# Kernel optimization log

Measured on AMD Instinct MI355X. Metric: run time of the kernel, lower is better.

Reference implementation:

```python
import jax, jax.numpy as jnp
import numpy as np

N = 100000
E = 1600000
F = 64
OUT = 7

def setup_inputs() -> dict:
    key = jax.random.key(0)
    k1, k2, k3, k4, k5 = jax.random.split(key, 5)
    x = jax.random.normal(k1, (N, F), dtype=jnp.float32)
    edge_index = jax.random.randint(k2, (2, E), 0, N, dtype=jnp.int64)
    W_l = jax.random.normal(k3, (F, OUT), dtype=jnp.float32) / np.sqrt(F)
    b_l = jax.random.normal(k4, (OUT,), dtype=jnp.float32) * 0.01
    W_r = jax.random.normal(k5, (F, OUT), dtype=jnp.float32) / np.sqrt(F)
    return {"x": x, "edge_index": edge_index, "W_l": W_l, "b_l": b_l, "W_r": W_r}

def reference(x, edge_index, W_l, b_l, W_r):
    # PyG SAGEConv (mean aggr): out = lin_l(mean_{j in N(i)} x_j) + lin_r(x_i), then relu
    src, dst = edge_index[0], edge_index[1]
    msgs = x[src]                                            # [E, F] gather
    agg = jax.ops.segment_sum(msgs, dst, num_segments=N)     # [N, F]
    cnt = jax.ops.segment_sum(jnp.ones((E,), dtype=x.dtype), dst, num_segments=N)
    mean = agg / jnp.maximum(cnt, 1.0)[:, None]              # isolated nodes -> 0
    out = mean @ W_l + b_l + x @ W_r                         # [N, 7]
    return jax.nn.relu(out)
```

## Files before the change

kernel.cpp:

```cpp
#include <hip/hip_runtime.h>

#define NN 100000
#define NE 1600000
#define FIN 64
#define FOUT 7

#define BSH 9
#define NBK 196
#define PBLK 2000
#define PTH  256
#define EPB  800
#define EPT  4
#define NCOPY 4
#define NCTR (NBK * NCOPY)
#define ROWS 200
#define SPLIT 2
#define RPS (PBLK / SPLIT)
#define ATH 1024
#define CAPR 8
#define OVCAP 256
#define SCAP 4608
#define PROJB 391
#define INVALID 0xFFFFFFFFu

__device__ __forceinline__ unsigned bf16r(float f) {
    unsigned u = __float_as_uint(f);
    return (u + 0x7fffu + ((u >> 16) & 1u)) >> 16;
}
__device__ __forceinline__ float bflo(unsigned u) { return __uint_as_float(u << 16); }
__device__ __forceinline__ float bfhi(unsigned u) { return __uint_as_float(u & 0xffff0000u); }

__global__ __launch_bounds__(256) void proj_kernel(
    const float* __restrict__ x, const float* __restrict__ Wl,
    const float* __restrict__ bl, const float* __restrict__ Wr,
    unsigned* __restrict__ z, float* __restrict__ outself, int n)
{
    int i = blockIdx.x * blockDim.x + threadIdx.x;
    if (i >= n) return;

    float al[FOUT], ar[FOUT];
#pragma unroll
    for (int j = 0; j < FOUT; ++j) { al[j] = 0.f; ar[j] = 0.f; }

    const float4* xr = (const float4*)(x + (size_t)i * FIN);
#pragma unroll
    for (int kk = 0; kk < FIN / 4; ++kk) {
        float4 xv = xr[kk];
        float v[4] = {xv.x, xv.y, xv.z, xv.w};
#pragma unroll
        for (int c = 0; c < 4; ++c) {
            int k = kk * 4 + c;
#pragma unroll
            for (int j = 0; j < FOUT; ++j) {
                al[j] = fmaf(v[c], Wl[k * FOUT + j], al[j]);
                ar[j] = fmaf(v[c], Wr[k * FOUT + j], ar[j]);
            }
        }
    }

    uint4 pk;
    pk.x = bf16r(al[0]) | (bf16r(al[1]) << 16);
    pk.y = bf16r(al[2]) | (bf16r(al[3]) << 16);
    pk.z = bf16r(al[4]) | (bf16r(al[5]) << 16);
    pk.w = bf16r(al[6]);
    ((uint4*)z)[i] = pk;

    float* o = outself + (size_t)i * FOUT;
#pragma unroll
    for (int j = 0; j < FOUT; ++j)
        o[j] = ar[j] + bl[j];
}

__global__ __launch_bounds__(PTH) void part_kernel(
    const int* __restrict__ eg, unsigned* __restrict__ part,
    unsigned short* __restrict__ offs)
{
    __shared__ unsigned st_cnt[NCTR];
    __shared__ unsigned st_start[NCTR];
    __shared__ unsigned wsum[NCOPY];

    const int t    = threadIdx.x;
    const int e0   = (int)blockIdx.x * EPB;
    const int lane = t & 63;
    const int wv   = t >> 6;

    for (int b = t; b < NCTR; b += PTH) st_cnt[b] = 0;
    __syncthreads();

    unsigned held[EPT], hcr[EPT];
#pragma unroll
    for (int j = 0; j < EPT; ++j) {
        int k = t + j * PTH;
        if (k < EPB) {
            unsigned s = (unsigned)eg[e0 + k];
            unsigned d = (unsigned)eg[NE + e0 + k];
            unsigned cidx = (d >> BSH) * NCOPY + wv;
            unsigned r = atomicAdd(&st_cnt[cidx], 1u);
            held[j] = ((d & 511u) << 17) | s;
            hcr[j]  = (cidx << 10) | r;
        } else hcr[j] = INVALID;
    }
    __syncthreads();

    {
        unsigned c[4], sum = 0;
#pragma unroll
        for (int q = 0; q < 4; ++q) {
            int idx = 4 * t + q;
            c[q] = (idx < NCTR) ? st_cnt[idx] : 0u;
            sum += c[q];
        }
        unsigned inc = sum;
#pragma unroll
        for (int off = 1; off < 64; off <<= 1) {
            unsigned v = (unsigned)__shfl_up((int)inc, off, 64);
            if (lane >= off) inc += v;
        }
        if (lane == 63) wsum[wv] = inc;
        __syncthreads();
        if (t == 0) {
            unsigned run = 0;
#pragma unroll
            for (int w = 0; w < NCOPY; ++w) { unsigned tmp = wsum[w]; wsum[w] = run; run += tmp; }
        }
        __syncthreads();
        unsigned base = wsum[wv] + inc - sum;
#pragma unroll
        for (int q = 0; q < 4; ++q) {
            int idx = 4 * t + q;
            if (idx < NCTR) st_start[idx] = base;
            base += c[q];
        }
    }
    __syncthreads();

    if (t <= NBK)
        offs[(size_t)blockIdx.x * ROWS + t] =
            (unsigned short)((t == NBK) ? EPB : st_start[t * NCOPY]);

    unsigned* pr = part + (size_t)blockIdx.x * EPB;
#pragma unroll
    for (int j = 0; j < EPT; ++j) {
        if (hcr[j] != INVALID) {
            unsigned cidx = hcr[j] >> 10, r = hcr[j] & 0x3FFu;
            pr[st_start[cidx] + r] = held[j];
        }
    }
}

__global__ __launch_bounds__(ATH) void acc_kernel(
    const unsigned short* __restrict__ offs, const unsigned* __restrict__ part,
    const unsigned* __restrict__ zb, float* __restrict__ partial)
{
    __shared__ unsigned s_cnt[512];
    __shared__ unsigned s_start[512];
    __shared__ unsigned sstage[SCAP];
    __shared__ float    lacc[512 * 8];
    __shared__ unsigned ovf[2 * OVCAP];
    __shared__ unsigned novf;
    __shared__ unsigned wtot[8];

    const int t = threadIdx.x;
    const int k = blockIdx.x >> 1;
    const int s = blockIdx.x & 1;

    if (t < 512) s_cnt[t] = 0;
    if (t == 0) novf = 0;
    __syncthreads();

    unsigned rbase = 0, len = 0;
    if (t < RPS) {
        unsigned r = (unsigned)(s * RPS + t);
        unsigned o0 = offs[(size_t)r * ROWS + k];
        unsigned o1 = offs[(size_t)r * ROWS + k + 1];
        len   = o1 - o0;
        rbase = r * EPB + o0;
    }

    unsigned hsrc[CAPR], hnr[CAPR];
#pragma unroll
    for (int j = 0; j < CAPR; ++j) {
        if (j < (int)len) {
            unsigned e = part[rbase + j];
            unsigned node = e >> 17;
            unsigned r = atomicAdd(&s_cnt[node], 1u);
            hsrc[j] = e & 0x1FFFFu;
            hnr[j]  = (node << 16) | r;
        } else hnr[j] = INVALID;
    }
    for (int j = CAPR; j < (int)len; ++j) {
        unsigned e = part[rbase + j];
        unsigned node = e >> 17;
        unsigned r = atomicAdd(&s_cnt[node], 1u);
        unsigned p = atomicAdd(&novf, 1u);
        if (p < OVCAP) {
            ovf[2 * p]     = (node << 16) | r;
            ovf[2 * p + 1] = e & 0x1FFFFu;
        }
    }
    __syncthreads();

    unsigned cval = 0, inc = 0;
    if (t < 512) {
        cval = s_cnt[t];
        inc = cval;
#pragma unroll
        for (int off = 1; off < 64; off <<= 1) {
            unsigned v = (unsigned)__shfl_up((int)inc, off, 64);
            if ((t & 63) >= off) inc += v;
        }
        if ((t & 63) == 63) wtot[t >> 6] = inc;
    }
    __syncthreads();
    if (t == 0) {
        unsigned run = 0;
#pragma unroll
        for (int w = 0; w < 8; ++w) { unsigned tmp = wtot[w]; wtot[w] = run; run += tmp; }
    }
    __syncthreads();
    if (t < 512) s_start[t] = wtot[t >> 6] + inc - cval;
    __syncthreads();

#pragma unroll
    for (int j = 0; j < CAPR; ++j) {
        if (hnr[j] != INVALID) {
            unsigned node = hnr[j] >> 16, r = hnr[j] & 0xffffu;
            unsigned p = s_start[node] + r;
            if (p < SCAP) sstage[p] = hsrc[j];
        }
    }
    for (unsigned q = t; q < min(novf, (unsigned)OVCAP); q += ATH) {
        unsigned nr = ovf[2 * q], src = ovf[2 * q + 1];
        unsigned p = s_start[nr >> 16] + (nr & 0xffffu);
        if (p < SCAP) sstage[p] = src;
    }
    __syncthreads();

    unsigned node = t & 511u;
    unsigned half = (unsigned)t >> 9;
    unsigned deg  = s_cnt[node];
    unsigned base = s_start[node];
    unsigned lo = half ? (deg >> 1) : 0u;
    unsigned hi = half ? deg : (deg >> 1);

    float a0 = 0.f, a1 = 0.f, a2 = 0.f, a3 = 0.f, a4 = 0.f, a5 = 0.f, a6 = 0.f;
    for (unsigned j = lo; j < hi && base + j < SCAP; ++j) {
        unsigned src = sstage[base + j];
        uint4 zr = ((const uint4*)zb)[src];
        a0 += bflo(zr.x); a1 += bfhi(zr.x);
        a2 += bflo(zr.y); a3 += bfhi(zr.y);
        a4 += bflo(zr.z); a5 += bfhi(zr.z);
        a6 += bflo(zr.w);
    }

    if (half) {
        float* L = &lacc[node * 8];
        *(float4*)(L)     = make_float4(a0, a1, a2, a3);
        *(float4*)(L + 4) = make_float4(a4, a5, a6, 0.f);
    }
    __syncthreads();

    if (!half) {
        const float* L = &lacc[node * 8];
        a0 += L[0]; a1 += L[1]; a2 += L[2]; a3 += L[3];
        a4 += L[4]; a5 += L[5]; a6 += L[6];
        float* pp = partial + ((size_t)blockIdx.x * 512 + node) * 8;
        *(float4*)(pp)     = make_float4(a0, a1, a2, a3);
        *(float4*)(pp + 4) = make_float4(a4, a5, a6, (float)deg);
    }
}

__global__ __launch_bounds__(256) void merge_kernel(
    const float* __restrict__ partial, float* __restrict__ out, int n)
{
    int i = blockIdx.x * blockDim.x + threadIdx.x;
    if (i >= n) return;
    int k = i >> BSH;
    int node = i & 511;

    float s0 = 0.f, s1 = 0.f, s2 = 0.f, s3 = 0.f, s4 = 0.f, s5 = 0.f, s6 = 0.f, cn = 0.f;
#pragma unroll
    for (int s = 0; s < SPLIT; ++s) {
        const float4* p = (const float4*)(partial + ((size_t)(k * SPLIT + s) * 512 + node) * 8);
        float4 a = p[0], b = p[1];
        s0 += a.x; s1 += a.y; s2 += a.z; s3 += a.w;
        s4 += b.x; s5 += b.y; s6 += b.z; cn += b.w;
    }
    float r = 1.0f / fmaxf(cn, 1.0f);
    float* o = out + (size_t)i * FOUT;
    o[0] = fmaxf(fmaf(s0, r, o[0]), 0.f);
    o[1] = fmaxf(fmaf(s1, r, o[1]), 0.f);
    o[2] = fmaxf(fmaf(s2, r, o[2]), 0.f);
    o[3] = fmaxf(fmaf(s3, r, o[3]), 0.f);
    o[4] = fmaxf(fmaf(s4, r, o[4]), 0.f);
    o[5] = fmaxf(fmaf(s5, r, o[5]), 0.f);
    o[6] = fmaxf(fmaf(s6, r, o[6]), 0.f);
}

extern "C" void kernel_launch(void* const* d_in, const int* in_sizes, int n_in,
                              void* d_out, int out_size, void* d_ws, size_t ws_size,
                              hipStream_t stream) {
    const float* x   = (const float*)d_in[0];
    const int*   edg = (const int*)d_in[1];
    const float* Wl  = (const float*)d_in[2];
    const float* bl  = (const float*)d_in[3];
    const float* Wr  = (const float*)d_in[4];
    float* out = (float*)d_out;

    unsigned*       z       = (unsigned*)d_ws;
    unsigned*       part    = z + (size_t)NN * 4;
    unsigned short* offs    = (unsigned short*)(part + (size_t)NE);
    float*          partial = (float*)(offs + (size_t)PBLK * ROWS);

    proj_kernel<<<PROJB, 256, 0, stream>>>(x, Wl, bl, Wr, z, out, NN);
    part_kernel<<<PBLK, PTH, 0, stream>>>(edg, part, offs);
    acc_kernel<<<NBK * SPLIT, ATH, 0, stream>>>(offs, part, z, partial);
    merge_kernel<<<(NN + 255) / 256, 256, 0, stream>>>(partial, out, NN);
}
```

Measured before the change: 127.1 us.

## Fuse four kernels into one persistent kernel with grid-wide barriers

Merges the projection, partition, accumulate and merge kernels into a single persistent kernel of 256 blocks of 1024 threads, with atomic-counter grid barriers between phases. This removes three kernel launches and their inter-kernel gaps. The partition step now stages edges in shared memory and writes them out coalesced as uint4. The accumulate split goes from 2 to 4 per bucket, with one thread per node and no half-split reduction. The cost is lower parallelism in each phase and spin-wait barrier overhead. The barrier also relies on all 256 blocks being co-resident, and it adds a memset launch.

```diff
diff --git a/kernel.cpp b/kernel.cpp
--- a/kernel.cpp
+++ b/kernel.cpp
@@ -7,20 +7,19 @@
 
 #define BSH 9
 #define NBK 196
-#define PBLK 2000
-#define PTH  256
+#define NREG 2000
 #define EPB  800
-#define EPT  4
+#define ROWS 200
 #define NCOPY 4
 #define NCTR (NBK * NCOPY)
-#define ROWS 200
-#define SPLIT 2
-#define RPS (PBLK / SPLIT)
-#define ATH 1024
+#define SPLIT 4
+#define NTASK (NBK * SPLIT)
+#define RPS (NREG / SPLIT)
 #define CAPR 8
 #define OVCAP 256
-#define SCAP 4608
-#define PROJB 391
+#define SCAP 2560
+#define BLKS 256
+#define TH 1024
 #define INVALID 0xFFFFFFFFu
 
 __device__ __forceinline__ unsigned bf16r(float f) {
@@ -30,271 +29,250 @@
 __device__ __forceinline__ float bflo(unsigned u) { return __uint_as_float(u << 16); }
 __device__ __forceinline__ float bfhi(unsigned u) { return __uint_as_float(u & 0xffff0000u); }
 
-__global__ __launch_bounds__(256) void proj_kernel(
-    const float* __restrict__ x, const float* __restrict__ Wl,
-    const float* __restrict__ bl, const float* __restrict__ Wr,
-    unsigned* __restrict__ z, float* __restrict__ outself, int n)
+__device__ __forceinline__ void gbarrier(int* cnt, int* gen) {
+    __syncthreads();
+    if (threadIdx.x == 0) {
+        int g = __hip_atomic_load(gen, __ATOMIC_ACQUIRE, __HIP_MEMORY_SCOPE_AGENT);
+        int a = __hip_atomic_fetch_add(cnt, 1, __ATOMIC_ACQ_REL, __HIP_MEMORY_SCOPE_AGENT);
+        if (a == BLKS - 1) {
+            __hip_atomic_store(cnt, 0, __ATOMIC_RELAXED, __HIP_MEMORY_SCOPE_AGENT);
+            __hip_atomic_fetch_add(gen, 1, __ATOMIC_ACQ_REL, __HIP_MEMORY_SCOPE_AGENT);
+        } else {
+            while (__hip_atomic_load(gen, __ATOMIC_ACQUIRE, __HIP_MEMORY_SCOPE_AGENT) == g)
+                __builtin_amdgcn_s_sleep(2);
+        }
+    }
+    __syncthreads();
+}
+
+__global__ __launch_bounds__(TH) void mega_kernel(
+    const int* __restrict__ eg, const float* __restrict__ x,
+    const float* __restrict__ Wl, const float* __restrict__ bl,
+    const float* __restrict__ Wr, unsigned* __restrict__ z,
+    unsigned* __restrict__ part, unsigned short* __restrict__ offs,
+    float* __restrict__ partial, float* __restrict__ out, int* __restrict__ bar)
 {
-    int i = blockIdx.x * blockDim.x + threadIdx.x;
-    if (i >= n) return;
-
-    float al[FOUT], ar[FOUT];
-#pragma unroll
-    for (int j = 0; j < FOUT; ++j) { al[j] = 0.f; ar[j] = 0.f; }
-
-    const float4* xr = (const float4*)(x + (size_t)i * FIN);
-#pragma unroll
-    for (int kk = 0; kk < FIN / 4; ++kk) {
-        float4 xv = xr[kk];
-        float v[4] = {xv.x, xv.y, xv.z, xv.w};
-#pragma unroll
-        for (int c = 0; c < 4; ++c) {
-            int k = kk * 4 + c;
-#pragma unroll
-            for (int j = 0; j < FOUT; ++j) {
-                al[j] = fmaf(v[c], Wl[k * FOUT + j], al[j]);
-                ar[j] = fmaf(v[c], Wr[k * FOUT + j], ar[j]);
-            }
-        }
-    }
-
-    uint4 pk;
-    pk.x = bf16r(al[0]) | (bf16r(al[1]) << 16);
-    pk.y = bf16r(al[2]) | (bf16r(al[3]) << 16);
-    pk.z = bf16r(al[4]) | (bf16r(al[5]) << 16);
-    pk.w = bf16r(al[6]);
-    ((uint4*)z)[i] = pk;
-
-    float* o = outself + (size_t)i * FOUT;
-#pragma unroll
-    for (int j = 0; j < FOUT; ++j)
-        o[j] = ar[j] + bl[j];
-}
-
-__global__ __launch_bounds__(PTH) void part_kernel(
-    const int* __restrict__ eg, unsigned* __restrict__ part,
-    unsigned short* __restrict__ offs)
-{
-    __shared__ unsigned st_cnt[NCTR];
-    __shared__ unsigned st_start[NCTR];
-    __shared__ unsigned wsum[NCOPY];
+    __shared__ unsigned s_cnt[NCTR];
+    __shared__ unsigned s_start[NCTR];
+    __shared__ unsigned sstage[SCAP];
+    __shared__ unsigned ovf[2 * OVCAP];
+    __shared__ unsigned novf;
+    __shared__ unsigned wtot[16];
 
     const int t    = threadIdx.x;
-    const int e0   = (int)blockIdx.x * EPB;
     const int lane = t & 63;
-    const int wv   = t >> 6;
-
-    for (int b = t; b < NCTR; b += PTH) st_cnt[b] = 0;
-    __syncthreads();
-
-    unsigned held[EPT], hcr[EPT];
-#pragma unroll
-    for (int j = 0; j < EPT; ++j) {
-        int k = t + j * PTH;
-        if (k < EPB) {
-            unsigned s = (unsigned)eg[e0 + k];
-            unsigned d = (unsigned)eg[NE + e0 + k];
-            unsigned cidx = (d >> BSH) * NCOPY + wv;
-            unsigned r = atomicAdd(&st_cnt[cidx], 1u);
-            held[j] = ((d & 511u) << 17) | s;
-            hcr[j]  = (cidx << 10) | r;
-        } else hcr[j] = INVALID;
-    }
-    __syncthreads();
 
     {
-        unsigned c[4], sum = 0;
-#pragma unroll
-        for (int q = 0; q < 4; ++q) {
-            int idx = 4 * t + q;
-            c[q] = (idx < NCTR) ? st_cnt[idx] : 0u;
-            sum += c[q];
-        }
-        unsigned inc = sum;
-#pragma unroll
-        for (int off = 1; off < 64; off <<= 1) {
-            unsigned v = (unsigned)__shfl_up((int)inc, off, 64);
-            if (lane >= off) inc += v;
-        }
-        if (lane == 63) wsum[wv] = inc;
+        int i = (int)blockIdx.x * TH + t;
+        if (i < NN) {
+            float al[FOUT], ar[FOUT];
+#pragma unroll
+            for (int j = 0; j < FOUT; ++j) { al[j] = 0.f; ar[j] = 0.f; }
+            const float4* xr = (const float4*)(x + (size_t)i * FIN);
+#pragma unroll
+            for (int kk = 0; kk < FIN / 4; ++kk) {
+                float4 xv = xr[kk];
+                float v[4] = {xv.x, xv.y, xv.z, xv.w};
+#pragma unroll
+                for (int c = 0; c < 4; ++c) {
+                    int k = kk * 4 + c;
+#pragma unroll
+                    for (int j = 0; j < FOUT; ++j) {
+                        al[j] = fmaf(v[c], Wl[k * FOUT + j], al[j]);
+                        ar[j] = fmaf(v[c], Wr[k * FOUT + j], ar[j]);
+                    }
+                }
+            }
+            uint4 pk;
+            pk.x = bf16r(al[0]) | (bf16r(al[1]) << 16);
+            pk.y = bf16r(al[2]) | (bf16r(al[3]) << 16);
+            pk.z = bf16r(al[4]) | (bf16r(al[5]) << 16);
+            pk.w = bf16r(al[6]);
+            ((uint4*)z)[i] = pk;
+            float* o = out + (size_t)i * FOUT;
+#pragma unroll
+            for (int j = 0; j < FOUT; ++j) o[j] = ar[j] + bl[j];
+        }
+    }
+
+    for (int r = blockIdx.x; r < NREG; r += BLKS) {
+        for (int i = t; i < NCTR; i += TH) s_cnt[i] = 0;
+        __syncthreads();
+
+        unsigned held = 0, hcr = INVALID;
+        if (t < EPB) {
+            unsigned s = (unsigned)eg[r * EPB + t];
+            unsigned d = (unsigned)eg[NE + r * EPB + t];
+            unsigned cidx = (d >> BSH) * NCOPY + ((t >> 6) & 3);
+            unsigned rk = atomicAdd(&s_cnt[cidx], 1u);
+            held = ((d & 511u) << 17) | s;
+            hcr  = (cidx << 10) | rk;
+        }
+        __syncthreads();
+
+        unsigned c0 = 0, c1 = 0, p = 0, inc = 0;
+        if (t < 512) {
+            unsigned i0 = 2 * t, i1 = 2 * t + 1;
+            c0 = (i0 < NCTR) ? s_cnt[i0] : 0u;
+            c1 = (i1 < NCTR) ? s_cnt[i1] : 0u;
+            p = c0 + c1; inc = p;
+#pragma unroll
+            for (int off = 1; off < 64; off <<= 1) {
+                unsigned v = (unsigned)__shfl_up((int)inc, off, 64);
+                if (lane >= off) inc += v;
+            }
+            if (lane == 63) wtot[t >> 6] = inc;
+        }
         __syncthreads();
         if (t == 0) {
             unsigned run = 0;
 #pragma unroll
-            for (int w = 0; w < NCOPY; ++w) { unsigned tmp = wsum[w]; wsum[w] = run; run += tmp; }
-        }
-        __syncthreads();
-        unsigned base = wsum[wv] + inc - sum;
-#pragma unroll
-        for (int q = 0; q < 4; ++q) {
-            int idx = 4 * t + q;
-            if (idx < NCTR) st_start[idx] = base;
-            base += c[q];
-        }
-    }
-    __syncthreads();
-
-    if (t <= NBK)
-        offs[(size_t)blockIdx.x * ROWS + t] =
-            (unsigned short)((t == NBK) ? EPB : st_start[t * NCOPY]);
-
-    unsigned* pr = part + (size_t)blockIdx.x * EPB;
-#pragma unroll
-    for (int j = 0; j < EPT; ++j) {
-        if (hcr[j] != INVALID) {
-            unsigned cidx = hcr[j] >> 10, r = hcr[j] & 0x3FFu;
-            pr[st_start[cidx] + r] = held[j];
-        }
-    }
-}
-
-__global__ __launch_bounds__(ATH) void acc_kernel(
-    const unsigned short* __restrict__ offs, const unsigned* __restrict__ part,
-    const unsigned* __restrict__ zb, float* __restrict__ partial)
-{
-    __shared__ unsigned s_cnt[512];
-    __shared__ unsigned s_start[512];
-    __shared__ unsigned sstage[SCAP];
-    __shared__ float    lacc[512 * 8];
-    __shared__ unsigned ovf[2 * OVCAP];
-    __shared__ unsigned novf;
-    __shared__ unsigned wtot[8];
-
-    const int t = threadIdx.x;
-    const int k = blockIdx.x >> 1;
-    const int s = blockIdx.x & 1;
-
-    if (t < 512) s_cnt[t] = 0;
-    if (t == 0) novf = 0;
-    __syncthreads();
-
-    unsigned rbase = 0, len = 0;
-    if (t < RPS) {
-        unsigned r = (unsigned)(s * RPS + t);
-        unsigned o0 = offs[(size_t)r * ROWS + k];
-        unsigned o1 = offs[(size_t)r * ROWS + k + 1];
-        len   = o1 - o0;
-        rbase = r * EPB + o0;
-    }
-
-    unsigned hsrc[CAPR], hnr[CAPR];
-#pragma unroll
-    for (int j = 0; j < CAPR; ++j) {
-        if (j < (int)len) {
+            for (int w = 0; w < 8; ++w) { unsigned tmp = wtot[w]; wtot[w] = run; run += tmp; }
+        }
+        __syncthreads();
+        if (t < 512) {
+            unsigned base = wtot[t >> 6] + inc - p;
+            unsigned i0 = 2 * t, i1 = 2 * t + 1;
+            if (i0 < NCTR) s_start[i0] = base;
+            if (i1 < NCTR) s_start[i1] = base + c0;
+        }
+        __syncthreads();
+
+        if (t <= NBK)
+            offs[(size_t)r * ROWS + t] =
+                (unsigned short)((t == NBK) ? EPB : s_start[t * NCOPY]);
+        if (hcr != INVALID)
+            sstage[s_start[hcr >> 10] + (hcr & 1023u)] = held;
+        __syncthreads();
+
+        uint4* pg = (uint4*)(part + (size_t)r * EPB);
+        if (t < EPB / 4) pg[t] = ((const uint4*)sstage)[t];
+        __syncthreads();
+    }
+
+    gbarrier(bar, bar + 16);
+
+    for (int task = blockIdx.x; task < NTASK; task += BLKS) {
+        const int k  = task >> 2;
+        const int sp = task & 3;
+
+        if (t < 512) s_cnt[t] = 0;
+        if (t == 0) novf = 0;
+        __syncthreads();
+
+        unsigned rbase = 0, len = 0;
+        if (t < RPS) {
+            unsigned r = (unsigned)(sp * RPS + t);
+            unsigned o0 = offs[(size_t)r * ROWS + k];
+            unsigned o1 = offs[(size_t)r * ROWS + k + 1];
+            len   = o1 - o0;
+            rbase = r * EPB + o0;
+        }
+
+        unsigned hsrc[CAPR], hnr[CAPR];
+#pragma unroll
+        for (int j = 0; j < CAPR; ++j) {
+            if (j < (int)len) {
+                unsigned e = part[rbase + j];
+                unsigned node = e >> 17;
+                unsigned rk = atomicAdd(&s_cnt[node], 1u);
+                hsrc[j] = e & 0x1FFFFu;
+                hnr[j]  = (node << 16) | rk;
+            } else hnr[j] = INVALID;
+        }
+        for (int j = CAPR; j < (int)len; ++j) {
             unsigned e = part[rbase + j];
             unsigned node = e >> 17;
-            unsigned r = atomicAdd(&s_cnt[node], 1u);
-            hsrc[j] = e & 0x1FFFFu;
-            hnr[j]  = (node << 16) | r;
-        } else hnr[j] = INVALID;
-    }
-    for (int j = CAPR; j < (int)len; ++j) {
-        unsigned e = part[rbase + j];
-        unsigned node = e >> 17;
-        unsigned r = atomicAdd(&s_cnt[node], 1u);
-        unsigned p = atomicAdd(&novf, 1u);
-        if (p < OVCAP) {
-            ovf[2 * p]     = (node << 16) | r;
-            ovf[2 * p + 1] = e & 0x1FFFFu;
-        }
-    }
-    __syncthreads();
-
-    unsigned cval = 0, inc = 0;
-    if (t < 512) {
-        cval = s_cnt[t];
-        inc = cval;
-#pragma unroll
-        for (int off = 1; off < 64; off <<= 1) {
-            unsigned v = (unsigned)__shfl_up((int)inc, off, 64);
-            if ((t & 63) >= off) inc += v;
-        }
-        if ((t & 63) == 63) wtot[t >> 6] = inc;
-    }
-    __syncthreads();
-    if (t == 0) {
-        unsigned run = 0;
-#pragma unroll
-        for (int w = 0; w < 8; ++w) { unsigned tmp = wtot[w]; wtot[w] = run; run += tmp; }
-    }
-    __syncthreads();
-    if (t < 512) s_start[t] = wtot[t >> 6] + inc - cval;
-    __syncthreads();
-
-#pragma unroll
-    for (int j = 0; j < CAPR; ++j) {
-        if (hnr[j] != INVALID) {
-            unsigned node = hnr[j] >> 16, r = hnr[j] & 0xffffu;
-            unsigned p = s_start[node] + r;
-            if (p < SCAP) sstage[p] = hsrc[j];
-        }
-    }
-    for (unsigned q = t; q < min(novf, (unsigned)OVCAP); q += ATH) {
-        unsigned nr = ovf[2 * q], src = ovf[2 * q + 1];
-        unsigned p = s_start[nr >> 16] + (nr & 0xffffu);
-        if (p < SCAP) sstage[p] = src;
-    }
-    __syncthreads();
-
-    unsigned node = t & 511u;
-    unsigned half = (unsigned)t >> 9;
-    unsigned deg  = s_cnt[node];
-    unsigned base = s_start[node];
-    unsigned lo = half ? (deg >> 1) : 0u;
-    unsigned hi = half ? deg : (deg >> 1);
-
-    float a0 = 0.f, a1 = 0.f, a2 = 0.f, a3 = 0.f, a4 = 0.f, a5 = 0.f, a6 = 0.f;
-    for (unsigned j = lo; j < hi && base + j < SCAP; ++j) {
-        unsigned src = sstage[base + j];
-        uint4 zr = ((const uint4*)zb)[src];
-        a0 += bflo(zr.x); a1 += bfhi(zr.x);
-        a2 += bflo(zr.y); a3 += bfhi(zr.y);
-        a4 += bflo(zr.z); a5 += bfhi(zr.z);
-        a6 += bflo(zr.w);
-    }
-
-    if (half) {
-        float* L = &lacc[node * 8];
-        *(float4*)(L)     = make_float4(a0, a1, a2, a3);
-        *(float4*)(L + 4) = make_float4(a4, a5, a6, 0.f);
-    }
-    __syncthreads();
-
-    if (!half) {
-        const float* L = &lacc[node * 8];
-        a0 += L[0]; a1 += L[1]; a2 += L[2]; a3 += L[3];
-        a4 += L[4]; a5 += L[5]; a6 += L[6];
-        float* pp = partial + ((size_t)blockIdx.x * 512 + node) * 8;
-        *(float4*)(pp)     = make_float4(a0, a1, a2, a3);
-        *(float4*)(pp + 4) = make_float4(a4, a5, a6, (float)deg);
-    }
-}
-
-__global__ __launch_bounds__(256) void merge_kernel(
-    const float* __restrict__ partial, float* __restrict__ out, int n)
-{
-    int i = blockIdx.x * blockDim.x + threadIdx.x;
-    if (i >= n) return;
-    int k = i >> BSH;
-    int node = i & 511;
-
-    float s0 = 0.f, s1 = 0.f, s2 = 0.f, s3 = 0.f, s4 = 0.f, s5 = 0.f, s6 = 0.f, cn = 0.f;
-#pragma unroll
-    for (int s = 0; s < SPLIT; ++s) {
-        const float4* p = (const float4*)(partial + ((size_t)(k * SPLIT + s) * 512 + node) * 8);
-        float4 a = p[0], b = p[1];
-        s0 += a.x; s1 += a.y; s2 += a.z; s3 += a.w;
-        s4 += b.x; s5 += b.y; s6 += b.z; cn += b.w;
-    }
-    float r = 1.0f / fmaxf(cn, 1.0f);
-    float* o = out + (size_t)i * FOUT;
-    o[0] = fmaxf(fmaf(s0, r, o[0]), 0.f);
-    o[1] = fmaxf(fmaf(s1, r, o[1]), 0.f);
-    o[2] = fmaxf(fmaf(s2, r, o[2]), 0.f);
-    o[3] = fmaxf(fmaf(s3, r, o[3]), 0.f);
-    o[4] = fmaxf(fmaf(s4, r, o[4]), 0.f);
-    o[5] = fmaxf(fmaf(s5, r, o[5]), 0.f);
-    o[6] = fmaxf(fmaf(s6, r, o[6]), 0.f);
+            unsigned rk = atomicAdd(&s_cnt[node], 1u);
+            unsigned pp = atomicAdd(&novf, 1u);
+            if (pp < OVCAP) {
+                ovf[2 * pp]     = (node << 16) | rk;
+                ovf[2 * pp + 1] = e & 0x1FFFFu;
+            }
+        }
+        __syncthreads();
+
+        unsigned cval = 0, inc = 0;
+        if (t < 512) {
+            cval = s_cnt[t]; inc = cval;
+#pragma unroll
+            for (int off = 1; off < 64; off <<= 1) {
+                unsigned v = (unsigned)__shfl_up((int)inc, off, 64);
+                if (lane >= off) inc += v;
+            }
+            if (lane == 63) wtot[t >> 6] = inc;
+        }
+        __syncthreads();
+        if (t == 0) {
+            unsigned run = 0;
+#pragma unroll
+            for (int w = 0; w < 8; ++w) { unsigned tmp = wtot[w]; wtot[w] = run; run += tmp; }
+        }
+        __syncthreads();
+        if (t < 512) s_start[t] = wtot[t >> 6] + inc - cval;
+        __syncthreads();
+
+#pragma unroll
+        for (int j = 0; j < CAPR; ++j) {
+            if (hnr[j] != INVALID) {
+                unsigned node = hnr[j] >> 16, rk = hnr[j] & 0xffffu;
+                unsigned pp = s_start[node] + rk;
+                if (pp < SCAP) sstage[pp] = hsrc[j];
+            }
+        }
+        for (unsigned q = t; q < min(novf, (unsigned)OVCAP); q += TH) {
+            unsigned nr = ovf[2 * q], src = ovf[2 * q + 1];
+            unsigned pp = s_start[nr >> 16] + (nr & 0xffffu);
+            if (pp < SCAP) sstage[pp] = src;
+        }
+        __syncthreads();
+
+        if (t < 512) {
+            unsigned deg  = s_cnt[t];
+            unsigned base = s_start[t];
+            unsigned hi   = min(base + deg, (unsigned)SCAP);
+            float a0 = 0.f, a1 = 0.f, a2 = 0.f, a3 = 0.f, a4 = 0.f, a5 = 0.f, a6 = 0.f;
+            for (unsigned j = base; j < hi; ++j) {
+                uint4 zr = ((const uint4*)z)[sstage[j]];
+                a0 += bflo(zr.x); a1 += bfhi(zr.x);
+                a2 += bflo(zr.y); a3 += bfhi(zr.y);
+                a4 += bflo(zr.z); a5 += bfhi(zr.z);
+                a6 += bflo(zr.w);
+            }
+            float* pp = partial + ((size_t)task * 512 + t) * 8;
+            *(float4*)(pp)     = make_float4(a0, a1, a2, a3);
+            *(float4*)(pp + 4) = make_float4(a4, a5, a6, (float)deg);
+        }
+        __syncthreads();
+    }
+
+    gbarrier(bar, bar + 16);
+
+    {
+        int i = (int)blockIdx.x * TH + t;
+        if (i < NN) {
+            int k = i >> BSH, node = i & 511;
+            float s0 = 0.f, s1 = 0.f, s2 = 0.f, s3 = 0.f,
+                  s4 = 0.f, s5 = 0.f, s6 = 0.f, cn = 0.f;
+#pragma unroll
+            for (int sp = 0; sp < SPLIT; ++sp) {
+                const float4* p =
+                    (const float4*)(partial + ((size_t)(k * SPLIT + sp) * 512 + node) * 8);
+                float4 a = p[0], b = p[1];
+                s0 += a.x; s1 += a.y; s2 += a.z; s3 += a.w;
+                s4 += b.x; s5 += b.y; s6 += b.z; cn += b.w;
+            }
+            float r = 1.0f / fmaxf(cn, 1.0f);
+            float* o = out + (size_t)i * FOUT;
+            o[0] = fmaxf(fmaf(s0, r, o[0]), 0.f);
+            o[1] = fmaxf(fmaf(s1, r, o[1]), 0.f);
+            o[2] = fmaxf(fmaf(s2, r, o[2]), 0.f);
+            o[3] = fmaxf(fmaf(s3, r, o[3]), 0.f);
+            o[4] = fmaxf(fmaf(s4, r, o[4]), 0.f);
+            o[5] = fmaxf(fmaf(s5, r, o[5]), 0.f);
+            o[6] = fmaxf(fmaf(s6, r, o[6]), 0.f);
+        }
+    }
 }
 
 extern "C" void kernel_launch(void* const* d_in, const int* in_sizes, int n_in,
@@ -310,10 +288,11 @@
     unsigned*       z       = (unsigned*)d_ws;
     unsigned*       part    = z + (size_t)NN * 4;
     unsigned short* offs    = (unsigned short*)(part + (size_t)NE);
-    float*          partial = (float*)(offs + (size_t)PBLK * ROWS);
-
-    proj_kernel<<<PROJB, 256, 0, stream>>>(x, Wl, bl, Wr, z, out, NN);
-    part_kernel<<<PBLK, PTH, 0, stream>>>(edg, part, offs);
-    acc_kernel<<<NBK * SPLIT, ATH, 0, stream>>>(offs, part, z, partial);
-    merge_kernel<<<(NN + 255) / 256, 256, 0, stream>>>(partial, out, NN);
-}
+    float*          partial = (float*)(offs + (size_t)NREG * ROWS);
+    int*            bar     = (int*)(partial + (size_t)NTASK * 512 * 8);
+
+    hipMemsetAsync(bar, 0, 32 * sizeof(int), stream);
+
+    mega_kernel<<<BLKS, TH, 0, stream>>>(edg, x, Wl, bl, Wr,
+                                         z, part, offs, partial, out, bar);
+}
```

After: 304.4 us. 2.39x slower.
